# Optimization experiments

Hardware: AMD Instinct MI355X
Metric: run time of the kernel (lower is better)

Reference implementation:

```python
import jax, jax.numpy as jnp
import numpy as np

T, N = 24, 2048
INPUT_DIM, HIDDEN, MEDIATE, SOCIAL, OUT_DIM = 2, 64, 128, 64, 2
N_SIZE = 2
CELL = 0.3
T_OBS, T_PRED = 9, 19
WIN = (N_SIZE + 1) ** 2  # (N_size+1)^2 = 9 window cells


def _social_pool(h, coords, mask):
    """Faithful social pooling for N_size=2, grid_cell_size=0.3.

    torch builds a dynamic grid, scatter-adds every agent's h into its cell,
    then gathers grid[int(x-R):int(x+R), int(y-R):int(y+R)] per agent.
    With R=0.3 and integer positions >= 4 (guaranteed by the margin), that
    slice is exactly the single cell (x-1, y-1), broadcast over the 3x3
    window. We compute it as a pairwise match without materializing a grid.
    Runs under torch.no_grad() -> stop_gradient.
    """
    margin = 2 * N_SIZE * CELL
    lt = jnp.stack([coords[:, 0].min(), coords[:, 1].min()]) - margin
    p = jnp.floor((coords - lt) / CELL).astype(jnp.int32)            # [N,2]
    p = p * mask.astype(jnp.int32)[:, None]                          # masked agents -> cell (0,0)
    q = p - 1                                                        # gathered cell per agent
    match = (p[None, :, 0] == q[:, None, 0]) & (p[None, :, 1] == q[:, None, 1])  # [i,j]
    cell_val = match.astype(h.dtype) @ h                             # [N,hidden] scatter-add + gather
    Hf = jnp.tile(cell_val, (1, WIN)) * mask[:, None]                # broadcast over 3x3 window, flat
    return jax.lax.stop_gradient(Hf)


def _forward(X, part_masks, all_h_t, all_c_t, Y, W_in, b_in, W_soc, b_soc,
             W_ih, W_hh, b_ih, b_hh, W_out, b_out, T_obs, T_pred):
    relu = jax.nn.relu  # dropout_prob = 0 -> Phi == ReLU

    def lstm(z, h, c):
        g = z @ W_ih.T + b_ih + h @ W_hh.T + b_hh
        i, f, gg, o = jnp.split(g, 4, axis=1)
        c = jax.nn.sigmoid(f) * c + jax.nn.sigmoid(i) * jnp.tanh(gg)
        h = jax.nn.sigmoid(o) * jnp.tanh(c)
        return h, c

    def cell_out(r, h, c, coords, m):
        Hf = _social_pool(h, coords, m)
        e = relu(Hf @ W_soc.T + b_soc)
        z = jnp.concatenate([r, e], axis=1)
        h, c = lstm(z, h, c)
        out = (h @ W_out.T + b_out) * m[:, None]
        return h, c, out

    def step_obs(carry, inp):
        h, c = carry
        x, m = inp
        r = relu(x @ W_in.T + b_in)
        h, c, out = cell_out(r, h, c, x, m)
        return (h, c), out

    (h, c), outs_obs = jax.lax.scan(
        step_obs, (all_h_t, all_c_t), (X[:T_obs + 1], part_masks[:T_obs + 1]))

    def step_pred(carry, inp):
        h, c, last_pt, prev_out = carry
        x, m = inp
        r = relu(last_pt @ W_in.T + b_in)
        h, c, out = cell_out(r, h, c, x, m)
        # torch: last_point = outputs[frame_idx - 1] AFTER the frame runs
        return (h, c, prev_out, out), out

    carry0 = (h, c, X[T_obs + 1], outs_obs[-1])
    _, outs_pred = jax.lax.scan(
        step_pred, carry0, (X[T_obs + 1:T_pred + 1], part_masks[T_obs + 1:T_pred + 1]))

    tail = jnp.zeros((X.shape[0] - T_pred - 1, X.shape[1], OUT_DIM), X.dtype)
    return jnp.concatenate([outs_obs, outs_pred, tail], axis=0)


def setup_inputs() -> dict:
    key = jax.random.key(0)
    ks = jax.random.split(key, 13)

    def lin(kw, kb, out_d, in_d):  # torch nn.Linear default init
        lim = 1.0 / float(np.sqrt(in_d))
        W = jax.random.uniform(kw, (out_d, in_d), minval=-lim, maxval=lim, dtype=jnp.float32)
        b = jax.random.uniform(kb, (out_d,), minval=-lim, maxval=lim, dtype=jnp.float32)
        return W, b

    W_in, b_in = lin(ks[0], ks[1], MEDIATE, INPUT_DIM)
    W_soc, b_soc = lin(ks[2], ks[3], SOCIAL, WIN * HIDDEN)
    W_ih, b_ih = lin(ks[4], ks[5], 4 * HIDDEN, MEDIATE + SOCIAL)
    W_hh, b_hh = lin(ks[6], ks[7], 4 * HIDDEN, HIDDEN)
    W_out, b_out = lin(ks[8], ks[9], OUT_DIM, HIDDEN)

    X = jax.random.normal(ks[10], (T, N, INPUT_DIM), dtype=jnp.float32) * 10.0  # meter-scale coords
    part_masks = (jax.random.uniform(ks[11], (T, N)) < 0.9).astype(jnp.float32)  # binary presence mask
    Y = jax.random.normal(ks[12], (T, N, INPUT_DIM), dtype=jnp.float32)  # unused by forward
    all_h_t = jnp.zeros((N, HIDDEN), jnp.float32)
    all_c_t = jnp.zeros((N, HIDDEN), jnp.float32)

    return {"X": X, "part_masks": part_masks, "all_h_t": all_h_t, "all_c_t": all_c_t,
            "Y": Y, "T_obs": T_OBS, "T_pred": T_PRED,
            "W_in": W_in, "b_in": b_in, "W_soc": W_soc, "b_soc": b_soc,
            "W_ih": W_ih, "W_hh": W_hh, "b_ih": b_ih, "b_hh": b_hh,
            "W_out": W_out, "b_out": b_out}


def reference(X, part_masks, all_h_t, all_c_t, Y, T_obs, T_pred,
              W_in, b_in, W_soc, b_soc, W_ih, W_hh, b_ih, b_hh, W_out, b_out):
    return _forward(X, part_masks, all_h_t, all_c_t, Y, W_in, b_in, W_soc, b_soc,
                    W_ih, W_hh, b_ih, b_hh, W_out, b_out, int(T_obs), int(T_pred))
```

## Files before the change

### kernel.cpp

```cpp
#include <hip/hip_runtime.h>
#include <math.h>


#define N_AG   2048
#define STEPS  20
#define CAP    12
#define NSRV   21
#define MAGIC  0x13572468

typedef short short8 __attribute__((ext_vector_type(8)));
typedef float f32x4  __attribute__((ext_vector_type(4)));
union FU { uint4 q; short8 v; };

__device__ __forceinline__ unsigned short bf16rne(float x) {
    unsigned u = __float_as_uint(x);
    unsigned r = (u + 0x7fff + ((u >> 16) & 1)) >> 16;
    return (unsigned short)r;
}

__device__ __forceinline__ void pack8(const float* v, uint4& hq, uint4& lq) {
    unsigned uh[4], ul[4];
    #pragma unroll
    for (int w = 0; w < 4; w++) {
        float v0 = v[2 * w], v1 = v[2 * w + 1];
        unsigned short h0 = bf16rne(v0), h1 = bf16rne(v1);
        float f0 = __uint_as_float(((unsigned)h0) << 16);
        float f1 = __uint_as_float(((unsigned)h1) << 16);
        unsigned short l0 = bf16rne(v0 - f0), l1 = bf16rne(v1 - f1);
        uh[w] = (unsigned)h0 | ((unsigned)h1 << 16);
        ul[w] = (unsigned)l0 | ((unsigned)l1 << 16);
    }
    hq = make_uint4(uh[0], uh[1], uh[2], uh[3]);
    lq = make_uint4(ul[0], ul[1], ul[2], ul[3]);
}

__device__ __forceinline__ int khash(int k) {
    return (int)(((unsigned)k * 2654435761u) >> 21);
}

__device__ __forceinline__ float fsigm(float x) {
    return __builtin_amdgcn_rcpf(1.f + __expf(-x));
}
__device__ __forceinline__ float ftanh(float x) {
    float e = __expf(2.f * x);
    return 1.f - 2.f * __builtin_amdgcn_rcpf(e + 1.f);
}

__device__ __forceinline__ void bar_lds() {
    asm volatile("s_waitcnt lgkmcnt(0)\n\ts_barrier" ::: "memory");
}

__device__ __forceinline__ void ast(int* p_, int v) {
    __hip_atomic_store(p_, v, __ATOMIC_RELAXED, __HIP_MEMORY_SCOPE_AGENT);
}
__device__ __forceinline__ void astf(float* p_, float v) {
    __hip_atomic_store(p_, v, __ATOMIC_RELAXED, __HIP_MEMORY_SCOPE_AGENT);
}
__device__ __forceinline__ unsigned long long aldu64(const unsigned long long* p_) {
    return __hip_atomic_load(p_, __ATOMIC_RELAXED, __HIP_MEMORY_SCOPE_AGENT);
}

struct KP {
    const float *X, *masks, *h_in, *c_in;
    const float *Win, *bin, *Wsoc, *bsoc, *Wih, *Whh, *bih, *bhh, *Wout, *bout;
    float *Wef;
    int *mcnt, *midx, *need, *flags;
    float *out;
    unsigned long long *hist;
};

__global__ __launch_bounds__(512, 1) void k_all(KP p)
{
    __shared__ __align__(16) uint4 zshq[544];
    __shared__ __align__(16) uint4 zslq[544];
    __shared__ float gbuf[16][258];
    __shared__ float cvs[16][64];
    __shared__ float hs[16][68];
    __shared__ float sWefP[64 * 65];
    __shared__ float2 sWinP[16 * 17];
    __shared__ float sBinP[16 * 9];
    __shared__ float sX[11][16][2];
    __shared__ float sMask[STEPS][16];
    __shared__ int   sCnt[STEPS][16];
    __shared__ int   sNeed[19][16];
    __shared__ int   sMidx[STEPS][16][CAP];
    __shared__ float sBsoc[64], sBc[256], sWout[128], sBout[2];
    __shared__ uint4 sE0h[8], sE0l[8];
    __shared__ int kk[N_AG];
    __shared__ int head[N_AG];
    __shared__ int nxt[N_AG];
    __shared__ float red[512];

    const int tid = threadIdx.x;
    const int bxg = blockIdx.x;

    if (bxg < NSRV) {
        const int sb = bxg;
        {
            int lo = sb * 780;
            int hi = (sb == NSRV - 1) ? 16384 : lo + 780;
            for (int i = lo + tid; i < hi; i += 512)
                p.out[20 * N_AG * 2 + i] = 0.f;
        }
        if (sb == 20) {
            for (int i = tid; i < 4096; i += 512) {
                int s = i >> 6, k = i & 63;
                float a = 0.f;
                #pragma unroll
                for (int w = 0; w < 9; w++) a += p.Wsoc[s * 576 + w * 64 + k];
                astf(&p.Wef[i], a);
            }
            __syncthreads();
            if (tid == 0) ast(&p.flags[20], MAGIC);
            return;
        }

        const int t = sb;
        const float* Xt = p.X + t * N_AG * 2;

        float mnx = 1e30f, mny = 1e30f;
        for (int i = tid; i < N_AG; i += 512) {
            mnx = fminf(mnx, Xt[2 * i]);
            mny = fminf(mny, Xt[2 * i + 1]);
        }
        red[tid] = mnx; __syncthreads();
        for (int s = 256; s > 0; s >>= 1) { if (tid < s) red[tid] = fminf(red[tid], red[tid + s]); __syncthreads(); }
        float ltx = red[0]; __syncthreads();
        red[tid] = mny; __syncthreads();
        for (int s = 256; s > 0; s >>= 1) { if (tid < s) red[tid] = fminf(red[tid], red[tid + s]); __syncthreads(); }
        float lty = red[0]; __syncthreads();
        ltx -= 1.2f;
        lty -= 1.2f;

        for (int i = tid; i < N_AG; i += 512) {
            float m = p.masks[t * N_AG + i];
            int px = (int)floorf((Xt[2 * i]     - ltx) / 0.3f);
            int py = (int)floorf((Xt[2 * i + 1] - lty) / 0.3f);
            int im = (int)m;
            px *= im; py *= im;
            kk[i] = px * 65536 + py;
            head[i] = -1;
            if (t >= 1) ast(&p.need[(t - 1) * N_AG + i], 0);
        }
        __syncthreads();
        for (int j = tid; j < N_AG; j += 512) {
            int kj = kk[j];
            if (kj != 0) nxt[j] = atomicExch(&head[khash(kj)], j);
        }
        __syncthreads();
        for (int i = tid; i < N_AG; i += 512) {
            int ki = kk[i];
            int cnt = 0;
            int base = (t * N_AG + i) * CAP;
            if (ki != 0) {
                int tkey = ki - 65537;
                int lst[CAP];
                for (int j = head[khash(tkey)]; j >= 0; j = nxt[j]) {
                    if (kk[j] == tkey) { if (cnt < CAP) lst[cnt] = j; cnt++; }
                }
                if (cnt > CAP) cnt = CAP;
                for (int a = 1; a < cnt; a++) {
                    int v = lst[a]; int b = a - 1;
                    while (b >= 0 && lst[b] > v) { lst[b + 1] = lst[b]; b--; }
                    lst[b + 1] = v;
                }
                for (int a = 0; a < cnt; a++) {
                    ast(&p.midx[base + a], lst[a]);
                    if (t >= 1) ast(&p.need[(t - 1) * N_AG + lst[a]], 1);
                }
            }
            ast(&p.mcnt[t * N_AG + i], cnt);
        }
        __syncthreads();
        if (tid == 0) ast(&p.flags[t], MAGIC);
        return;
    }

    const int bx    = bxg - NSRV;
    const int wbase = bx * 16;
    const int wv    = tid >> 6, lane = tid & 63;
    const int mA    = lane & 15, quad = lane >> 4;
    const int nt0   = 2 * wv;
    const int m0w   = wv, m1w = wv + 8;

    if (tid < 256) sBc[tid] = p.bih[tid] + p.bhh[tid];
    if (tid < 128) {
        sWout[tid] = p.Wout[tid];
        int c = tid;
        sWinP[(c >> 3) * 17 + (c & 7)] = make_float2(p.Win[2 * c], p.Win[2 * c + 1]);
        sBinP[(c >> 3) * 9 + (c & 7)] = p.bin[c];
    }
    if (tid < 64) sBsoc[tid] = p.bsoc[tid];
    if (tid < 2)  sBout[tid] = p.bout[tid];
    if (tid < 8) {
        float v[8];
        #pragma unroll
        for (int j = 0; j < 8; j++) v[j] = fmaxf(p.bsoc[tid * 8 + j], 0.f);
        pack8(v, sE0h[tid], sE0l[tid]);
    }
    if (tid < 352) { int tt = tid / 32, r = tid % 32;
                     sX[tt][r >> 1][r & 1] = p.X[tt * (N_AG * 2) + (wbase + (r >> 1)) * 2 + (r & 1)]; }
    if (tid < 320) { int tt = tid / 16, m2 = tid % 16;
                     sMask[tt][m2] = p.masks[tt * N_AG + wbase + m2]; }

    float c0, c1;
    {
        hs[m0w][lane] = p.h_in[(wbase + m0w) * 64 + lane];
        hs[m1w][lane] = p.h_in[(wbase + m1w) * 64 + lane];
        c0 = p.c_in[(wbase + m0w) * 64 + lane];
        c1 = p.c_in[(wbase + m1w) * 64 + lane];
    }

    FU wh[2][8], wl[2][8];
    #pragma unroll
    for (int e = 0; e < 2; e++) {
        int g = (nt0 + e) * 16 + mA;
        #pragma unroll
        for (int kt = 0; kt < 8; kt++) {
            int k0 = kt * 32 + quad * 8;
            const float* src = (k0 < 192) ? (p.Wih + g * 192 + k0)
                                          : (p.Whh + g * 64 + (k0 - 192));
            float v[8];
            #pragma unroll
            for (int j = 0; j < 8; j++) v[j] = src[j];
            pack8(v, wh[e][kt].q, wl[e][kt].q);
        }
    }

    if (tid < NSRV) {
        while (__hip_atomic_load(&p.flags[tid], __ATOMIC_RELAXED,
                                 __HIP_MEMORY_SCOPE_AGENT) != MAGIC) { }
    }
    __syncthreads();

    if (tid < 320) { int tt = tid / 16, m2 = tid % 16;
                     sCnt[tt][m2] = p.mcnt[tt * N_AG + wbase + m2]; }
    if (tid < 304) { int s = tid / 16, m2 = tid % 16;
                     sNeed[s][m2] = p.need[s * N_AG + wbase + m2]; }
    for (int i = tid; i < 4096; i += 512) sWefP[(i >> 6) * 65 + (i & 63)] = p.Wef[i];
    for (int i = tid; i < STEPS * 16 * CAP; i += 512) {
        int tt = i / (16 * CAP), r = i % (16 * CAP), m2 = r / CAP, n = r % CAP;
        sMidx[tt][m2][n] = p.midx[(tt * N_AG + wbase + m2) * CAP + n];
    }
    __syncthreads();

    {
        if (lane < 32) {
            int a = lane & 1, s5r = lane >> 1;
            int m = a ? m1w : m0w;
            float px = sX[0][m][0], py = sX[0][m][1];
            float v[8];
            #pragma unroll
            for (int j = 0; j < 8; j++) {
                float2 w2 = sWinP[s5r * 17 + j];
                v[j] = fmaxf(w2.x * px + w2.y * py + sBinP[s5r * 9 + j], 0.f);
            }
            pack8(v, zshq[s5r * 17 + m], zslq[s5r * 17 + m]);
        } else if (lane < 48) {
            int idx = lane - 32, a = idx & 1, s58 = idx >> 1;
            int m = a ? m1w : m0w;
            float v[8];
            #pragma unroll
            for (int j = 0; j < 8; j++) v[j] = hs[m][s58 * 8 + j];
            pack8(v, zshq[(24 + s58) * 17 + m], zslq[(24 + s58) * 17 + m]);
        } else {
            int idx = lane - 48, a = idx & 1, s58 = idx >> 1;
            int m = a ? m1w : m0w;
            if (sCnt[0][m] == 0) {
                zshq[(16 + s58) * 17 + m] = sE0h[s58];
                zslq[(16 + s58) * 17 + m] = sE0l[s58];
            }
        }
    }
    bar_lds();

    float op0x = 0.f, op0y = 0.f, op1x = 0.f, op1y = 0.f;

    #pragma unroll 1
    for (int t = 0; t < STEPS; t++) {
        const int m5 = tid >> 5, s5 = tid & 31;
        const int cnt5 = sCnt[t][m5];

        const unsigned long long* hb = p.hist + (size_t)(t - 1) * (N_AG * 64);
        unsigned long long pw0 = 0, pw1 = 0, qw0 = 0, qw1 = 0;
        int rfirst = -1, rsecond = -1;
        if (cnt5 > 0 && t > 0) {
            rfirst = sMidx[t][m5][0];
            pw0 = aldu64(&hb[rfirst * 64 + s5]);
            pw1 = aldu64(&hb[rfirst * 64 + s5 + 32]);
            if (cnt5 > 1) {
                rsecond = sMidx[t][m5][1];
                qw0 = aldu64(&hb[rsecond * 64 + s5]);
                qw1 = aldu64(&hb[rsecond * 64 + s5 + 32]);
            }
        }

        f32x4 a0v = {0.f, 0.f, 0.f, 0.f};
        f32x4 a1v = {0.f, 0.f, 0.f, 0.f};
        #pragma unroll
        for (int u = 0; u < 6; u++) {
            const int kt = (u < 4) ? u : u + 2;
            int fi = (kt * 4 + quad) * 17 + mA;
            FU az, bz;
            az.q = zshq[fi];
            bz.q = zslq[fi];
            a0v = __builtin_amdgcn_mfma_f32_16x16x32_bf16(az.v, wh[0][kt].v, a0v, 0, 0, 0);
            a1v = __builtin_amdgcn_mfma_f32_16x16x32_bf16(az.v, wh[1][kt].v, a1v, 0, 0, 0);
            a0v = __builtin_amdgcn_mfma_f32_16x16x32_bf16(bz.v, wh[0][kt].v, a0v, 0, 0, 0);
            a1v = __builtin_amdgcn_mfma_f32_16x16x32_bf16(bz.v, wh[1][kt].v, a1v, 0, 0, 0);
            a0v = __builtin_amdgcn_mfma_f32_16x16x32_bf16(az.v, wl[0][kt].v, a0v, 0, 0, 0);
            a1v = __builtin_amdgcn_mfma_f32_16x16x32_bf16(az.v, wl[1][kt].v, a1v, 0, 0, 0);
        }

        if (cnt5 > 0) {
            float a0 = 0.f, a1 = 0.f;
            if (t == 0) {
                for (int n = 0; n < cnt5; n++) {
                    int r = sMidx[0][m5][n];
                    a0 += p.h_in[r * 64 + s5];
                    a1 += p.h_in[r * 64 + s5 + 32];
                }
            } else {
                const unsigned tagw = (unsigned)t;
                while ((unsigned)(pw0 >> 32) != tagw || (unsigned)(pw1 >> 32) != tagw) {
                    pw0 = aldu64(&hb[rfirst * 64 + s5]);
                    pw1 = aldu64(&hb[rfirst * 64 + s5 + 32]);
                }
                a0 += __uint_as_float((unsigned)pw0);
                a1 += __uint_as_float((unsigned)pw1);
                if (cnt5 > 1) {
                    while ((unsigned)(qw0 >> 32) != tagw || (unsigned)(qw1 >> 32) != tagw) {
                        qw0 = aldu64(&hb[rsecond * 64 + s5]);
                        qw1 = aldu64(&hb[rsecond * 64 + s5 + 32]);
                    }
                    a0 += __uint_as_float((unsigned)qw0);
                    a1 += __uint_as_float((unsigned)qw1);
                    for (int n = 2; n < cnt5; n++) {
                        int r = sMidx[t][m5][n];
                        unsigned long long w0, w1;
                        do {
                            w0 = aldu64(&hb[r * 64 + s5]);
                            w1 = aldu64(&hb[r * 64 + s5 + 32]);
                        } while ((unsigned)(w0 >> 32) != tagw || (unsigned)(w1 >> 32) != tagw);
                        a0 += __uint_as_float((unsigned)w0);
                        a1 += __uint_as_float((unsigned)w1);
                    }
                }
            }
            cvs[m5][s5] = a0; cvs[m5][s5 + 32] = a1;
            float acc0 = sBsoc[s5], acc1 = sBsoc[s5 + 32];
            const float* w0p = &sWefP[s5 * 65];
            const float* w1p = &sWefP[(s5 + 32) * 65];
            for (int k = 0; k < 64; k++) {
                float cv = cvs[m5][k];
                acc0 += cv * w0p[k];
                acc1 += cv * w1p[k];
            }
            acc0 = fmaxf(acc0, 0.f);
            acc1 = fmaxf(acc1, 0.f);
            const int base = (m5 & 1) * 32;
            float v[8];
            #pragma unroll
            for (int jj = 0; jj < 8; jj++) {
                int c = s5 * 8 + jj;
                int srcl = base + ((c < 32 ? c : c - 32) & 31);
                float va = __shfl(acc0, srcl, 64);
                float vb = __shfl(acc1, srcl, 64);
                v[jj] = (c < 32) ? va : vb;
            }
            if (s5 < 8)
                pack8(v, zshq[(16 + s5) * 17 + m5], zslq[(16 + s5) * 17 + m5]);
        }
        bar_lds();

        #pragma unroll
        for (int kt = 4; kt <= 5; kt++) {
            int fi = (kt * 4 + quad) * 17 + mA;
            FU az, bz;
            az.q = zshq[fi];
            bz.q = zslq[fi];
            a0v = __builtin_amdgcn_mfma_f32_16x16x32_bf16(az.v, wh[0][kt].v, a0v, 0, 0, 0);
            a1v = __builtin_amdgcn_mfma_f32_16x16x32_bf16(az.v, wh[1][kt].v, a1v, 0, 0, 0);
            a0v = __builtin_amdgcn_mfma_f32_16x16x32_bf16(bz.v, wh[0][kt].v, a0v, 0, 0, 0);
            a1v = __builtin_amdgcn_mfma_f32_16x16x32_bf16(bz.v, wh[1][kt].v, a1v, 0, 0, 0);
            a0v = __builtin_amdgcn_mfma_f32_16x16x32_bf16(az.v, wl[0][kt].v, a0v, 0, 0, 0);
            a1v = __builtin_amdgcn_mfma_f32_16x16x32_bf16(az.v, wl[1][kt].v, a1v, 0, 0, 0);
        }
        #pragma unroll
        for (int r = 0; r < 4; r++) {
            int row = quad * 4 + r;
            gbuf[row][nt0 * 16 + mA]       = a0v[r];
            gbuf[row][(nt0 + 1) * 16 + mA] = a1v[r];
        }
        bar_lds();

        {
            const int hid = lane;
            float hn0, hn1;
            {
                float gi = gbuf[m0w][hid]       + sBc[hid];
                float gf = gbuf[m0w][64 + hid]  + sBc[64 + hid];
                float gR = gbuf[m0w][128 + hid] + sBc[128 + hid];
                float go = gbuf[m0w][192 + hid] + sBc[192 + hid];
                float cn = fsigm(gf) * c0 + fsigm(gi) * ftanh(gR);
                hn0 = fsigm(go) * ftanh(cn);
                c0 = cn;
                hs[m0w][hid] = hn0;
            }
            {
                float gi = gbuf[m1w][hid]       + sBc[hid];
                float gf = gbuf[m1w][64 + hid]  + sBc[64 + hid];
                float gR = gbuf[m1w][128 + hid] + sBc[128 + hid];
                float go = gbuf[m1w][192 + hid] + sBc[192 + hid];
                float cn = fsigm(gf) * c1 + fsigm(gi) * ftanh(gR);
                hn1 = fsigm(go) * ftanh(cn);
                c1 = cn;
                hs[m1w][hid] = hn1;
            }
            if (t <= 18) {
                unsigned long long* hp = p.hist + (size_t)t * (N_AG * 64);
                unsigned long long tg = ((unsigned long long)(t + 1)) << 32;
                if (sNeed[t][m0w])
                    __hip_atomic_store(&hp[(wbase + m0w) * 64 + hid],
                                       tg | (unsigned long long)__float_as_uint(hn0),
                                       __ATOMIC_RELAXED, __HIP_MEMORY_SCOPE_AGENT);
                if (sNeed[t][m1w])
                    __hip_atomic_store(&hp[(wbase + m1w) * 64 + hid],
                                       tg | (unsigned long long)__float_as_uint(hn1),
                                       __ATOMIC_RELAXED, __HIP_MEMORY_SCOPE_AGENT);
            }

            float w0 = sWout[hid], w1 = sWout[64 + hid];
            float p00 = hn0 * w0, p01 = hn0 * w1;
            float p10 = hn1 * w0, p11 = hn1 * w1;
            #pragma unroll
            for (int off = 32; off >= 1; off >>= 1) {
                p00 += __shfl_xor(p00, off);
                p01 += __shfl_xor(p01, off);
                p10 += __shfl_xor(p10, off);
                p11 += __shfl_xor(p11, off);
            }
            float mk0 = sMask[t][m0w], mk1 = sMask[t][m1w];
            float o00 = (p00 + sBout[0]) * mk0, o01 = (p01 + sBout[1]) * mk0;
            float o10 = (p10 + sBout[0]) * mk1, o11 = (p11 + sBout[1]) * mk1;
            if (lane == 0)
                *(float2*)&p.out[(t * N_AG + wbase + m0w) * 2] = make_float2(o00, o01);
            if (lane == 1)
                *(float2*)&p.out[(t * N_AG + wbase + m1w) * 2] = make_float2(o10, o11);

            if (t < STEPS - 1) {
                const int tn = t + 1;
                if (lane < 32) {
                    int a = lane & 1, s5r = lane >> 1;
                    int m = a ? m1w : m0w;
                    float px, py;
                    if (tn <= 10) { px = sX[tn][m][0]; py = sX[tn][m][1]; }
                    else          { px = a ? op1x : op0x;
                                    py = a ? op1y : op0y; }
                    float v[8];
                    #pragma unroll
                    for (int j = 0; j < 8; j++) {
                        float2 w2 = sWinP[s5r * 17 + j];
                        v[j] = fmaxf(w2.x * px + w2.y * py + sBinP[s5r * 9 + j], 0.f);
                    }
                    pack8(v, zshq[s5r * 17 + m], zslq[s5r * 17 + m]);
                } else if (lane < 48) {
                    int idx = lane - 32, a = idx & 1, s58 = idx >> 1;
                    int m = a ? m1w : m0w;
                    float v[8];
                    #pragma unroll
                    for (int j = 0; j < 8; j++) v[j] = hs[m][s58 * 8 + j];
                    pack8(v, zshq[(24 + s58) * 17 + m], zslq[(24 + s58) * 17 + m]);
                } else {
                    int idx = lane - 48, a = idx & 1, s58 = idx >> 1;
                    int m = a ? m1w : m0w;
                    if (sCnt[tn][m] == 0) {
                        zshq[(16 + s58) * 17 + m] = sE0h[s58];
                        zslq[(16 + s58) * 17 + m] = sE0l[s58];
                    }
                }
            }
            op0x = o00; op0y = o01;
            op1x = o10; op1y = o11;
        }
        bar_lds();
    }
}

extern "C" void kernel_launch(void* const* d_in, const int* in_sizes, int n_in,
                              void* d_out, int out_size, void* d_ws, size_t ws_size,
                              hipStream_t stream)
{
    KP kp;
    kp.X     = (const float*)d_in[0];
    kp.masks = (const float*)d_in[1];
    kp.h_in  = (const float*)d_in[2];
    kp.c_in  = (const float*)d_in[3];
    kp.Win   = (const float*)d_in[7];
    kp.bin   = (const float*)d_in[8];
    kp.Wsoc  = (const float*)d_in[9];
    kp.bsoc  = (const float*)d_in[10];
    kp.Wih   = (const float*)d_in[11];
    kp.Whh   = (const float*)d_in[12];
    kp.bih   = (const float*)d_in[13];
    kp.bhh   = (const float*)d_in[14];
    kp.Wout  = (const float*)d_in[15];
    kp.bout  = (const float*)d_in[16];
    kp.out   = (float*)d_out;

    unsigned long long* hist = (unsigned long long*)d_ws;
    float* Wef  = (float*)(hist + 19 * N_AG * 64);
    int*   need = (int*)(Wef + 4096);
    int*   mcnt = need + 19 * N_AG;
    int*   midx = mcnt + STEPS * N_AG;
    int*   flags = midx + STEPS * N_AG * CAP;

    kp.hist = hist; kp.Wef = Wef; kp.need = need; kp.mcnt = mcnt;
    kp.midx = midx; kp.flags = flags;

    k_all<<<NSRV + 128, 512, 0, stream>>>(kp);
}
```

Before: 184.5 us.

## Move social pooling gather to end of previous step and merge MFMA passes

The neighbour-hidden gather and the social embedding dot product for step t+1 now run at the tail of step t, right after the hidden state is published, rather than at the start of step t. This removes one block barrier per step and lets a single 8-tile MFMA loop replace the split 6+2 passes. The cross-block wait moves earlier in the step, so it may block on slower blocks sooner. The bf16 hi/lo split now uses the packed v_cvt_pk_bf16_f32 instruction, and the embedding dot product is unrolled with float4 LDS reads.

```diff
diff --git a/kernel.cpp b/kernel.cpp
--- a/kernel.cpp
+++ b/kernel.cpp
@@ -12,23 +12,19 @@
 typedef float f32x4  __attribute__((ext_vector_type(4)));
 union FU { uint4 q; short8 v; };
 
-__device__ __forceinline__ unsigned short bf16rne(float x) {
-    unsigned u = __float_as_uint(x);
-    unsigned r = (u + 0x7fff + ((u >> 16) & 1)) >> 16;
-    return (unsigned short)r;
-}
-
 __device__ __forceinline__ void pack8(const float* v, uint4& hq, uint4& lq) {
     unsigned uh[4], ul[4];
     #pragma unroll
     for (int w = 0; w < 4; w++) {
         float v0 = v[2 * w], v1 = v[2 * w + 1];
-        unsigned short h0 = bf16rne(v0), h1 = bf16rne(v1);
-        float f0 = __uint_as_float(((unsigned)h0) << 16);
-        float f1 = __uint_as_float(((unsigned)h1) << 16);
-        unsigned short l0 = bf16rne(v0 - f0), l1 = bf16rne(v1 - f1);
-        uh[w] = (unsigned)h0 | ((unsigned)h1 << 16);
-        ul[w] = (unsigned)l0 | ((unsigned)l1 << 16);
+        unsigned h;
+        asm("v_cvt_pk_bf16_f32 %0, %1, %2" : "=v"(h) : "v"(v0), "v"(v1));
+        float f0 = __uint_as_float(h << 16);
+        float f1 = __uint_as_float(h & 0xffff0000u);
+        float r0 = v0 - f0, r1 = v1 - f1;
+        unsigned l;
+        asm("v_cvt_pk_bf16_f32 %0, %1, %2" : "=v"(l) : "v"(r0), "v"(r1));
+        uh[w] = h; ul[w] = l;
     }
     hq = make_uint4(uh[0], uh[1], uh[2], uh[3]);
     lq = make_uint4(ul[0], ul[1], ul[2], ul[3]);
@@ -58,6 +54,43 @@
 }
 __device__ __forceinline__ unsigned long long aldu64(const unsigned long long* p_) {
     return __hip_atomic_load(p_, __ATOMIC_RELAXED, __HIP_MEMORY_SCOPE_AGENT);
+}
+
+__device__ __forceinline__ void edot_frag(
+    int m5, int s5, float a0, float a1,
+    float (*cvs)[68], const float* sWefP, const float* sBsoc,
+    uint4* zshq, uint4* zslq)
+{
+    cvs[m5][s5] = a0; cvs[m5][s5 + 32] = a1;
+    float acc0 = sBsoc[s5],       acc1 = sBsoc[s5 + 32];
+    float acc0b = 0.f,            acc1b = 0.f;
+    const float* w0p = &sWefP[s5 * 65];
+    const float* w1p = &sWefP[(s5 + 32) * 65];
+    const float4* cw = (const float4*)&cvs[m5][0];
+    #pragma unroll
+    for (int k4 = 0; k4 < 16; k4 += 2) {
+        float4 ca = cw[k4];
+        float4 cb = cw[k4 + 1];
+        int k = k4 * 4;
+        acc0  += ca.x * w0p[k]     + ca.y * w0p[k + 1] + ca.z * w0p[k + 2] + ca.w * w0p[k + 3];
+        acc1  += ca.x * w1p[k]     + ca.y * w1p[k + 1] + ca.z * w1p[k + 2] + ca.w * w1p[k + 3];
+        acc0b += cb.x * w0p[k + 4] + cb.y * w0p[k + 5] + cb.z * w0p[k + 6] + cb.w * w0p[k + 7];
+        acc1b += cb.x * w1p[k + 4] + cb.y * w1p[k + 5] + cb.z * w1p[k + 6] + cb.w * w1p[k + 7];
+    }
+    acc0 = fmaxf(acc0 + acc0b, 0.f);
+    acc1 = fmaxf(acc1 + acc1b, 0.f);
+    const int base = (m5 & 1) * 32;
+    float v[8];
+    #pragma unroll
+    for (int jj = 0; jj < 8; jj++) {
+        int c = s5 * 8 + jj;
+        int srcl = base + ((c < 32 ? c : c - 32) & 31);
+        float va = __shfl(acc0, srcl, 64);
+        float vb = __shfl(acc1, srcl, 64);
+        v[jj] = (c < 32) ? va : vb;
+    }
+    if (s5 < 8)
+        pack8(v, zshq[(16 + s5) * 17 + m5], zslq[(16 + s5) * 17 + m5]);
 }
 
 struct KP {
@@ -74,8 +107,8 @@
     __shared__ __align__(16) uint4 zshq[544];
     __shared__ __align__(16) uint4 zslq[544];
     __shared__ float gbuf[16][258];
-    __shared__ float cvs[16][64];
-    __shared__ float hs[16][68];
+    __shared__ __align__(16) float cvs[16][68];
+    __shared__ __align__(16) float hs[16][68];
     __shared__ float sWefP[64 * 65];
     __shared__ float2 sWinP[16 * 17];
     __shared__ float sBinP[16 * 9];
@@ -182,6 +215,7 @@
     const int mA    = lane & 15, quad = lane >> 4;
     const int nt0   = 2 * wv;
     const int m0w   = wv, m1w = wv + 8;
+    const int m5    = tid >> 5, s5 = tid & 31;
 
     if (tid < 256) sBc[tid] = p.bih[tid] + p.bhh[tid];
     if (tid < 128) {
@@ -271,6 +305,16 @@
                 zslq[(16 + s58) * 17 + m] = sE0l[s58];
             }
         }
+        int cnt0 = sCnt[0][m5];
+        if (cnt0 > 0) {
+            float a0 = 0.f, a1 = 0.f;
+            for (int n = 0; n < cnt0; n++) {
+                int r = sMidx[0][m5][n];
+                a0 += p.h_in[r * 64 + s5];
+                a1 += p.h_in[r * 64 + s5 + 32];
+            }
+            edot_frag(m5, s5, a0, a1, cvs, sWefP, sBsoc, zshq, zslq);
+        }
     }
     bar_lds();
 
@@ -278,103 +322,10 @@
 
     #pragma unroll 1
     for (int t = 0; t < STEPS; t++) {
-        const int m5 = tid >> 5, s5 = tid & 31;
-        const int cnt5 = sCnt[t][m5];
-
-        const unsigned long long* hb = p.hist + (size_t)(t - 1) * (N_AG * 64);
-        unsigned long long pw0 = 0, pw1 = 0, qw0 = 0, qw1 = 0;
-        int rfirst = -1, rsecond = -1;
-        if (cnt5 > 0 && t > 0) {
-            rfirst = sMidx[t][m5][0];
-            pw0 = aldu64(&hb[rfirst * 64 + s5]);
-            pw1 = aldu64(&hb[rfirst * 64 + s5 + 32]);
-            if (cnt5 > 1) {
-                rsecond = sMidx[t][m5][1];
-                qw0 = aldu64(&hb[rsecond * 64 + s5]);
-                qw1 = aldu64(&hb[rsecond * 64 + s5 + 32]);
-            }
-        }
-
         f32x4 a0v = {0.f, 0.f, 0.f, 0.f};
         f32x4 a1v = {0.f, 0.f, 0.f, 0.f};
         #pragma unroll
-        for (int u = 0; u < 6; u++) {
-            const int kt = (u < 4) ? u : u + 2;
-            int fi = (kt * 4 + quad) * 17 + mA;
-            FU az, bz;
-            az.q = zshq[fi];
-            bz.q = zslq[fi];
-            a0v = __builtin_amdgcn_mfma_f32_16x16x32_bf16(az.v, wh[0][kt].v, a0v, 0, 0, 0);
-            a1v = __builtin_amdgcn_mfma_f32_16x16x32_bf16(az.v, wh[1][kt].v, a1v, 0, 0, 0);
-            a0v = __builtin_amdgcn_mfma_f32_16x16x32_bf16(bz.v, wh[0][kt].v, a0v, 0, 0, 0);
-            a1v = __builtin_amdgcn_mfma_f32_16x16x32_bf16(bz.v, wh[1][kt].v, a1v, 0, 0, 0);
-            a0v = __builtin_amdgcn_mfma_f32_16x16x32_bf16(az.v, wl[0][kt].v, a0v, 0, 0, 0);
-            a1v = __builtin_amdgcn_mfma_f32_16x16x32_bf16(az.v, wl[1][kt].v, a1v, 0, 0, 0);
-        }
-
-        if (cnt5 > 0) {
-            float a0 = 0.f, a1 = 0.f;
-            if (t == 0) {
-                for (int n = 0; n < cnt5; n++) {
-                    int r = sMidx[0][m5][n];
-                    a0 += p.h_in[r * 64 + s5];
-                    a1 += p.h_in[r * 64 + s5 + 32];
-                }
-            } else {
-                const unsigned tagw = (unsigned)t;
-                while ((unsigned)(pw0 >> 32) != tagw || (unsigned)(pw1 >> 32) != tagw) {
-                    pw0 = aldu64(&hb[rfirst * 64 + s5]);
-                    pw1 = aldu64(&hb[rfirst * 64 + s5 + 32]);
-                }
-                a0 += __uint_as_float((unsigned)pw0);
-                a1 += __uint_as_float((unsigned)pw1);
-                if (cnt5 > 1) {
-                    while ((unsigned)(qw0 >> 32) != tagw || (unsigned)(qw1 >> 32) != tagw) {
-                        qw0 = aldu64(&hb[rsecond * 64 + s5]);
-                        qw1 = aldu64(&hb[rsecond * 64 + s5 + 32]);
-                    }
-                    a0 += __uint_as_float((unsigned)qw0);
-                    a1 += __uint_as_float((unsigned)qw1);
-                    for (int n = 2; n < cnt5; n++) {
-                        int r = sMidx[t][m5][n];
-                        unsigned long long w0, w1;
-                        do {
-                            w0 = aldu64(&hb[r * 64 + s5]);
-                            w1 = aldu64(&hb[r * 64 + s5 + 32]);
-                        } while ((unsigned)(w0 >> 32) != tagw || (unsigned)(w1 >> 32) != tagw);
-                        a0 += __uint_as_float((unsigned)w0);
-                        a1 += __uint_as_float((unsigned)w1);
-                    }
-                }
-            }
-            cvs[m5][s5] = a0; cvs[m5][s5 + 32] = a1;
-            float acc0 = sBsoc[s5], acc1 = sBsoc[s5 + 32];
-            const float* w0p = &sWefP[s5 * 65];
-            const float* w1p = &sWefP[(s5 + 32) * 65];
-            for (int k = 0; k < 64; k++) {
-                float cv = cvs[m5][k];
-                acc0 += cv * w0p[k];
-                acc1 += cv * w1p[k];
-            }
-            acc0 = fmaxf(acc0, 0.f);
-            acc1 = fmaxf(acc1, 0.f);
-            const int base = (m5 & 1) * 32;
-            float v[8];
-            #pragma unroll
-            for (int jj = 0; jj < 8; jj++) {
-                int c = s5 * 8 + jj;
-                int srcl = base + ((c < 32 ? c : c - 32) & 31);
-                float va = __shfl(acc0, srcl, 64);
-                float vb = __shfl(acc1, srcl, 64);
-                v[jj] = (c < 32) ? va : vb;
-            }
-            if (s5 < 8)
-                pack8(v, zshq[(16 + s5) * 17 + m5], zslq[(16 + s5) * 17 + m5]);
-        }
-        bar_lds();
-
-        #pragma unroll
-        for (int kt = 4; kt <= 5; kt++) {
+        for (int kt = 0; kt < 8; kt++) {
             int fi = (kt * 4 + quad) * 17 + mA;
             FU az, bz;
             az.q = zshq[fi];
@@ -428,6 +379,23 @@
                     __hip_atomic_store(&hp[(wbase + m1w) * 64 + hid],
                                        tg | (unsigned long long)__float_as_uint(hn1),
                                        __ATOMIC_RELAXED, __HIP_MEMORY_SCOPE_AGENT);
+            }
+
+            const unsigned long long* hb = p.hist + (size_t)t * (N_AG * 64);
+            int cntN = 0, rfirst = -1, rsecond = -1;
+            unsigned long long pw0 = 0, pw1 = 0, qw0 = 0, qw1 = 0;
+            if (t < STEPS - 1) {
+                cntN = sCnt[t + 1][m5];
+                if (cntN > 0) {
+                    rfirst = sMidx[t + 1][m5][0];
+                    pw0 = aldu64(&hb[rfirst * 64 + s5]);
+                    pw1 = aldu64(&hb[rfirst * 64 + s5 + 32]);
+                    if (cntN > 1) {
+                        rsecond = sMidx[t + 1][m5][1];
+                        qw0 = aldu64(&hb[rsecond * 64 + s5]);
+                        qw1 = aldu64(&hb[rsecond * 64 + s5 + 32]);
+                    }
+                }
             }
 
             float w0 = sWout[hid], w1 = sWout[64 + hid];
@@ -467,9 +435,9 @@
                 } else if (lane < 48) {
                     int idx = lane - 32, a = idx & 1, s58 = idx >> 1;
                     int m = a ? m1w : m0w;
-                    float v[8];
-                    #pragma unroll
-                    for (int j = 0; j < 8; j++) v[j] = hs[m][s58 * 8 + j];
+                    const float4* hr = (const float4*)&hs[m][s58 * 8];
+                    float4 h0 = hr[0], h1 = hr[1];
+                    float v[8] = { h0.x, h0.y, h0.z, h0.w, h1.x, h1.y, h1.z, h1.w };
                     pack8(v, zshq[(24 + s58) * 17 + m], zslq[(24 + s58) * 17 + m]);
                 } else {
                     int idx = lane - 48, a = idx & 1, s58 = idx >> 1;
@@ -480,6 +448,36 @@
                     }
                 }
             }
+
+            if (cntN > 0) {
+                const unsigned tagw = (unsigned)(t + 1);
+                while ((unsigned)(pw0 >> 32) != tagw || (unsigned)(pw1 >> 32) != tagw) {
+                    pw0 = aldu64(&hb[rfirst * 64 + s5]);
+                    pw1 = aldu64(&hb[rfirst * 64 + s5 + 32]);
+                }
+                float a0 = __uint_as_float((unsigned)pw0);
+                float a1 = __uint_as_float((unsigned)pw1);
+                if (cntN > 1) {
+                    while ((unsigned)(qw0 >> 32) != tagw || (unsigned)(qw1 >> 32) != tagw) {
+                        qw0 = aldu64(&hb[rsecond * 64 + s5]);
+                        qw1 = aldu64(&hb[rsecond * 64 + s5 + 32]);
+                    }
+                    a0 += __uint_as_float((unsigned)qw0);
+                    a1 += __uint_as_float((unsigned)qw1);
+                    for (int n = 2; n < cntN; n++) {
+                        int r = sMidx[t + 1][m5][n];
+                        unsigned long long w0_, w1_;
+                        do {
+                            w0_ = aldu64(&hb[r * 64 + s5]);
+                            w1_ = aldu64(&hb[r * 64 + s5 + 32]);
+                        } while ((unsigned)(w0_ >> 32) != tagw || (unsigned)(w1_ >> 32) != tagw);
+                        a0 += __uint_as_float((unsigned)w0_);
+                        a1 += __uint_as_float((unsigned)w1_);
+                    }
+                }
+                edot_frag(m5, s5, a0, a1, cvs, sWefP, sBsoc, zshq, zslq);
+            }
+
             op0x = o00; op0y = o01;
             op1x = o10; op1y = o11;
         }
```

After: 178.6 us. 3.2% less time.
